# Kernel tuning notes

Hardware: AMD Instinct MI355X
Metric: run time of the kernel (lower is better)

Reference implementation:

```python
import jax, jax.numpy as jnp
import numpy as np

N_NODES = 50000
N_EDGES = 800000
HIDDEN = 128
MAX_Z = 1000
NUM_GRAPHS = 1000
NODES_PER_GRAPH = N_NODES // NUM_GRAPHS


def setup_inputs() -> dict:
    key = jax.random.key(0)
    ks = jax.random.split(key, 12)
    s = 1.0 / np.sqrt(HIDDEN)
    inp = {
        "z": jax.random.randint(ks[0], (N_NODES,), 0, MAX_Z),
        "edge_index": jax.random.randint(ks[1], (2, N_EDGES), 0, N_NODES),
        # sorted batch ids, 50 nodes per graph (SEAL-style subgraph batch)
        "batch": jnp.repeat(jnp.arange(NUM_GRAPHS), NODES_PER_GRAPH),
        "num_graphs": NUM_GRAPHS,
        "emb_table": jax.random.normal(ks[2], (MAX_Z, HIDDEN), jnp.float32),
        "w0": jax.random.normal(ks[3], (HIDDEN, HIDDEN), jnp.float32) * s,
        "b0": jnp.zeros((HIDDEN,), jnp.float32),
        "w1": jax.random.normal(ks[4], (HIDDEN, HIDDEN), jnp.float32) * s,
        "b1": jnp.zeros((HIDDEN,), jnp.float32),
        "w2": jax.random.normal(ks[5], (HIDDEN, HIDDEN), jnp.float32) * s,
        "b2": jnp.zeros((HIDDEN,), jnp.float32),
        "lin1_w": jax.random.normal(ks[6], (HIDDEN, HIDDEN), jnp.float32) * s,
        "lin1_b": jnp.zeros((HIDDEN,), jnp.float32),
        "lin2_w": jax.random.normal(ks[7], (HIDDEN, 1), jnp.float32) * s,
        "lin2_b": jnp.zeros((1,), jnp.float32),
    }
    return inp


def reference(z, edge_index, batch, num_graphs, emb_table, w0, b0, w1, b1, w2, b2,
              lin1_w, lin1_b, lin2_w, lin2_b):
    n = z.shape[0]
    # GCN symmetric normalization with self-loops (PyG gcn_norm, edge_weight=1)
    loops = jnp.arange(n)
    src = jnp.concatenate([edge_index[0], loops])
    dst = jnp.concatenate([edge_index[1], loops])
    ones = jnp.ones(src.shape[0], dtype=emb_table.dtype)
    deg = jax.ops.segment_sum(ones, dst, num_segments=n)
    dinv = jnp.where(deg > 0, jax.lax.rsqrt(deg), 0.0)
    norm = dinv[src] * dinv[dst]  # [E+N]

    def gcn_conv(x, W, b):
        h = x @ W  # linear transform first (bias added after aggregation)
        msg = h[src] * norm[:, None]  # gather + scale over edges
        return jax.ops.segment_sum(msg, dst, num_segments=n) + b

    x = emb_table[z]  # z embedding (z is 1-D -> no sum over dim 1)
    # dropout is identity in eval mode
    x = jax.nn.relu(gcn_conv(x, w0, b0))
    x = jax.nn.relu(gcn_conv(x, w1, b1))
    x = gcn_conv(x, w2, b2)

    # first occurrence of each batch id (batch is sorted per PyG convention)
    center = jax.ops.segment_min(jnp.arange(n), batch, num_segments=num_graphs)
    g = x[center] * x[center + 1]  # [G, H] pairwise link readout
    g = jax.nn.relu(g @ lin1_w + lin1_b)
    return g @ lin2_w + lin2_b  # [G, 1]
```

## Files before the change

### kernel.cpp

```cpp
#include <hip/hip_runtime.h>
#include <hip/hip_fp16.h>
#include <cstdint>
#include <cstddef>

#define H 128

typedef _Float16 f16x8 __attribute__((ext_vector_type(8)));
typedef float f32x4 __attribute__((ext_vector_type(4)));

__device__ inline float2 up2(unsigned u) {
    return __half22float2(*reinterpret_cast<const __half2*>(&u));
}
__device__ inline unsigned pk2(float a, float b) {
    __half2 h = __floats2half2_rn(a, b);
    return *reinterpret_cast<unsigned*>(&h);
}

__global__ void init_kernel(int* __restrict__ fill, int n,
                            const float* __restrict__ w0, const float* __restrict__ w1,
                            const float* __restrict__ w2, _Float16* __restrict__ wt) {
    int idx = blockIdx.x * 256 + threadIdx.x;
    if (idx < n) fill[idx] = 0;
    if (idx < 3 * H * H) {
        int m = idx >> 14;
        int c = (idx >> 7) & 127;
        int k = idx & 127;
        const float* W = (m == 0) ? w0 : (m == 1) ? w1 : w2;
        wt[idx] = (_Float16)W[k * H + c];
    }
}

__global__ __launch_bounds__(256) void fill_xcd(const int* __restrict__ src,
                                                const int* __restrict__ dst, int E,
                                                int* __restrict__ fill,
                                                unsigned short* __restrict__ csr_pad,
                                                int n, int rs) {
    int p = blockIdx.x & 7;
    int lo = p * rs;
    int hi = lo + rs; if (hi > n) hi = n;
    int nchunks = gridDim.x >> 3;
    int chunk = blockIdx.x >> 3;
    int stride = nchunks * 256;
    int E4 = E >> 2;
    const int4* dst4 = reinterpret_cast<const int4*>(dst);

    for (int q = chunk * 256 + threadIdx.x; q < E4; q += stride) {
        int4 d4 = dst4[q];
        int e = q * 4;
        if (d4.x >= lo && d4.x < hi) {
            int s = src[e];
            int pos = atomicAdd(&fill[d4.x], 1);
            if (pos < 64) csr_pad[(d4.x << 6) + pos] = (unsigned short)s;
        }
        if (d4.y >= lo && d4.y < hi) {
            int s = src[e + 1];
            int pos = atomicAdd(&fill[d4.y], 1);
            if (pos < 64) csr_pad[(d4.y << 6) + pos] = (unsigned short)s;
        }
        if (d4.z >= lo && d4.z < hi) {
            int s = src[e + 2];
            int pos = atomicAdd(&fill[d4.z], 1);
            if (pos < 64) csr_pad[(d4.z << 6) + pos] = (unsigned short)s;
        }
        if (d4.w >= lo && d4.w < hi) {
            int s = src[e + 3];
            int pos = atomicAdd(&fill[d4.w], 1);
            if (pos < 64) csr_pad[(d4.w << 6) + pos] = (unsigned short)s;
        }
    }
    if (blockIdx.x < 8) {
        int e = E4 * 4 + threadIdx.x;
        if (e < E) {
            int d = dst[e];
            if (d >= lo && d < hi) {
                int s = src[e];
                int pos = atomicAdd(&fill[d], 1);
                if (pos < 64) csr_pad[(d << 6) + pos] = (unsigned short)s;
            }
        }
    }
}

__global__ void post_fill(const int* __restrict__ fill, float* __restrict__ dinv,
                          const int* __restrict__ batch, int* __restrict__ sel, int n) {
    int i = blockIdx.x * 256 + threadIdx.x;
    if (i < n) {
        dinv[i] = rsqrtf((float)(fill[i] + 1));
        int b = batch[i];
        if (i == 0 || batch[i - 1] != b) {
            sel[2 * b] = i;
            sel[2 * b + 1] = (i + 1 < n) ? i + 1 : n - 1;
        }
    }
}


template<int MODE>
__global__ __launch_bounds__(256) void gemm_mfma(const void* __restrict__ Xv,
                                                 const int* __restrict__ z,
                                                 const _Float16* __restrict__ Wt,
                                                 unsigned* __restrict__ Yh, int n) {
    __shared__ _Float16 Wl[H * H];
    __shared__ _Float16 Cl[64 * H];
    int tid = threadIdx.x;

    {
        const uint4* src = reinterpret_cast<const uint4*>(Wt);
        #pragma unroll
        for (int it = 0; it < 8; ++it) {
            int idx = it * 256 + tid;
            int c = idx >> 4, s = idx & 15;
            unsigned boff = (unsigned)(c * 256 + s * 16) ^ ((unsigned)(c & 7) << 4);
            *reinterpret_cast<uint4*>(reinterpret_cast<char*>(Wl) + boff) = src[idx];
        }
    }

    int m0 = blockIdx.x * 64;
    int wid = tid >> 6, lane = tid & 63;
    int l15 = lane & 15, lhi = lane >> 4;
    int grow = m0 + wid * 16 + l15;
    bool rowok = grow < n;

    const float* xrow32 = nullptr;
    const _Float16* xrow16 = nullptr;
    if (MODE == 0) {
        const float* X = (const float*)Xv;
        int zr = rowok ? z[grow] : 0;
        xrow32 = X + (size_t)zr * H;
    } else {
        const _Float16* X = (const _Float16*)Xv;
        xrow16 = X + (size_t)(rowok ? grow : 0) * H;
    }

    unsigned braw[8];
    unsigned swz = (unsigned)(l15 & 7) << 4;
    #pragma unroll
    for (int ct = 0; ct < 8; ++ct) {
        int c = ct * 16 + l15;
        braw[ct] = (unsigned)(c * 256 + lhi * 16);
    }

    f32x4 acc[8];
    #pragma unroll
    for (int ct = 0; ct < 8; ++ct) acc[ct] = (f32x4){0.f, 0.f, 0.f, 0.f};

    __syncthreads();

    #pragma unroll
    for (int kb = 0; kb < 4; ++kb) {
        f16x8 a;
        if (MODE == 0) {
            const float* ap = xrow32 + kb * 32 + lhi * 8;
            float4 x0 = *reinterpret_cast<const float4*>(ap);
            float4 x1 = *reinterpret_cast<const float4*>(ap + 4);
            a[0] = (_Float16)x0.x; a[1] = (_Float16)x0.y;
            a[2] = (_Float16)x0.z; a[3] = (_Float16)x0.w;
            a[4] = (_Float16)x1.x; a[5] = (_Float16)x1.y;
            a[6] = (_Float16)x1.z; a[7] = (_Float16)x1.w;
        } else {
            a = *reinterpret_cast<const f16x8*>(xrow16 + kb * 32 + lhi * 8);
        }
        #pragma unroll
        for (int ct = 0; ct < 8; ++ct) {
            unsigned boff = (braw[ct] + (unsigned)(kb * 64)) ^ swz;
            f16x8 b = *reinterpret_cast<const f16x8*>(
                reinterpret_cast<const char*>(Wl) + boff);
            acc[ct] = __builtin_amdgcn_mfma_f32_16x16x32_f16(a, b, acc[ct], 0, 0, 0);
        }
    }

    _Float16* cw = Cl + wid * 16 * H;
    #pragma unroll
    for (int ct = 0; ct < 8; ++ct) {
        #pragma unroll
        for (int r = 0; r < 4; ++r) {
            int row = lhi * 4 + r;
            int col = ct * 16 + l15;
            cw[row * H + col] = (_Float16)acc[ct][r];
        }
    }
    int orow = lane >> 2, oseg = lane & 3;
    int growo = m0 + wid * 16 + orow;
    if (growo < n) {
        const uint4* cp = reinterpret_cast<const uint4*>(
            reinterpret_cast<const char*>(cw) + orow * 256 + oseg * 64);
        uint4* dp = reinterpret_cast<uint4*>(
            reinterpret_cast<char*>(Yh) + (size_t)growo * 256 + oseg * 64);
        dp[0] = cp[0]; dp[1] = cp[1]; dp[2] = cp[2]; dp[3] = cp[3];
    }
}


__device__ inline float4 agg_core(const unsigned* __restrict__ Hb,
                                  const unsigned short* __restrict__ csr_pad,
                                  const float* __restrict__ dinv,
                                  const float* __restrict__ bias,
                                  int node, int deg, float di,
                                  int lane, int half, int l32) {
    const uint2* Hu = reinterpret_cast<const uint2*>(Hb);
    float4 acc0 = make_float4(0.f, 0.f, 0.f, 0.f);
    float4 acc1 = make_float4(0.f, 0.f, 0.f, 0.f);
    float4 acc2 = make_float4(0.f, 0.f, 0.f, 0.f);
    float4 acc3 = make_float4(0.f, 0.f, 0.f, 0.f);
    if (half == 0) {
        float s = di * di;
        uint2 u = Hu[(size_t)node * 32 + l32];
        float4 bv = reinterpret_cast<const float4*>(bias)[l32];
        float2 f0 = up2(u.x), f1 = up2(u.y);
        acc0.x = bv.x + f0.x * s;
        acc0.y = bv.y + f0.y * s;
        acc0.z = bv.z + f1.x * s;
        acc0.w = bv.w + f1.y * s;
    }
    int beg = node << 6;
    int end = beg + deg;
    int j = beg + half;
    for (; j + 6 < end; j += 8) {
        int s0 = csr_pad[j];
        int s1 = csr_pad[j + 2];
        int s2 = csr_pad[j + 4];
        int s3 = csr_pad[j + 6];
        uint2 u0 = Hu[(size_t)s0 * 32 + l32];
        uint2 u1 = Hu[(size_t)s1 * 32 + l32];
        uint2 u2 = Hu[(size_t)s2 * 32 + l32];
        uint2 u3 = Hu[(size_t)s3 * 32 + l32];
        float n0 = dinv[s0] * di;
        float n1 = dinv[s1] * di;
        float n2 = dinv[s2] * di;
        float n3 = dinv[s3] * di;
        float2 a0 = up2(u0.x), b0 = up2(u0.y);
        float2 a1 = up2(u1.x), b1 = up2(u1.y);
        float2 a2 = up2(u2.x), b2 = up2(u2.y);
        float2 a3 = up2(u3.x), b3 = up2(u3.y);
        acc0.x = fmaf(a0.x, n0, acc0.x); acc0.y = fmaf(a0.y, n0, acc0.y);
        acc0.z = fmaf(b0.x, n0, acc0.z); acc0.w = fmaf(b0.y, n0, acc0.w);
        acc1.x = fmaf(a1.x, n1, acc1.x); acc1.y = fmaf(a1.y, n1, acc1.y);
        acc1.z = fmaf(b1.x, n1, acc1.z); acc1.w = fmaf(b1.y, n1, acc1.w);
        acc2.x = fmaf(a2.x, n2, acc2.x); acc2.y = fmaf(a2.y, n2, acc2.y);
        acc2.z = fmaf(b2.x, n2, acc2.z); acc2.w = fmaf(b2.y, n2, acc2.w);
        acc3.x = fmaf(a3.x, n3, acc3.x); acc3.y = fmaf(a3.y, n3, acc3.y);
        acc3.z = fmaf(b3.x, n3, acc3.z); acc3.w = fmaf(b3.y, n3, acc3.w);
    }
    for (; j < end; j += 2) {
        int s0 = csr_pad[j];
        uint2 u0 = Hu[(size_t)s0 * 32 + l32];
        float n0 = dinv[s0] * di;
        float2 a0 = up2(u0.x), b0 = up2(u0.y);
        acc0.x = fmaf(a0.x, n0, acc0.x); acc0.y = fmaf(a0.y, n0, acc0.y);
        acc0.z = fmaf(b0.x, n0, acc0.z); acc0.w = fmaf(b0.y, n0, acc0.w);
    }
    acc0.x += acc1.x + acc2.x + acc3.x;
    acc0.y += acc1.y + acc2.y + acc3.y;
    acc0.z += acc1.z + acc2.z + acc3.z;
    acc0.w += acc1.w + acc2.w + acc3.w;
    acc0.x += __shfl_xor(acc0.x, 32);
    acc0.y += __shfl_xor(acc0.y, 32);
    acc0.z += __shfl_xor(acc0.z, 32);
    acc0.w += __shfl_xor(acc0.w, 32);
    return acc0;
}

__global__ __launch_bounds__(256) void agg_f16(const unsigned* __restrict__ Hb,
                                               const int* __restrict__ degc,
                                               const unsigned short* __restrict__ csr_pad,
                                               const float* __restrict__ dinv,
                                               const float* __restrict__ bias,
                                               unsigned* __restrict__ Out, int n) {
    int node = blockIdx.x * 4 + (threadIdx.x >> 6);
    if (node >= n) return;
    int lane = threadIdx.x & 63;
    int half = lane >> 5, l32 = lane & 31;
    int deg = degc[node]; if (deg > 64) deg = 64;
    float di = dinv[node];
    float4 a = agg_core(Hb, csr_pad, dinv, bias, node, deg, di, lane, half, l32);
    if (half == 0) {
        a.x = fmaxf(a.x, 0.f); a.y = fmaxf(a.y, 0.f);
        a.z = fmaxf(a.z, 0.f); a.w = fmaxf(a.w, 0.f);
        uint2 pv; pv.x = pk2(a.x, a.y); pv.y = pk2(a.z, a.w);
        reinterpret_cast<uint2*>(Out)[(size_t)node * 32 + l32] = pv;
    }
}

__global__ __launch_bounds__(256) void agg_sel(const unsigned* __restrict__ Hb,
                                               const int* __restrict__ degc,
                                               const unsigned short* __restrict__ csr_pad,
                                               const float* __restrict__ dinv,
                                               const float* __restrict__ bias,
                                               const int* __restrict__ sel,
                                               float* __restrict__ Out, int nSel) {
    int idx = blockIdx.x * 4 + (threadIdx.x >> 6);
    if (idx >= nSel) return;
    int node = sel[idx];
    int lane = threadIdx.x & 63;
    int half = lane >> 5, l32 = lane & 31;
    int deg = degc[node]; if (deg > 64) deg = 64;
    float di = dinv[node];
    float4 a = agg_core(Hb, csr_pad, dinv, bias, node, deg, di, lane, half, l32);
    if (half == 0)
        reinterpret_cast<float4*>(Out)[(size_t)idx * 32 + l32] = a;
}


__global__ __launch_bounds__(128) void readout_kernel(const float* __restrict__ OSel,
                                                      const float* __restrict__ w1,
                                                      const float* __restrict__ b1,
                                                      const float* __restrict__ w2,
                                                      const float* __restrict__ b2,
                                                      float* __restrict__ out) {
    __shared__ float gv[H];
    __shared__ float red[H];
    int g = blockIdx.x;
    int c = threadIdx.x;
    gv[c] = OSel[(size_t)(2 * g) * H + c] * OSel[(size_t)(2 * g + 1) * H + c];
    __syncthreads();
    float acc = b1[c];
    #pragma unroll 8
    for (int k = 0; k < H; ++k)
        acc = fmaf(gv[k], w1[k * H + c], acc);
    acc = fmaxf(acc, 0.f);
    red[c] = acc * w2[c];
    __syncthreads();
    for (int off = 64; off > 0; off >>= 1) {
        if (c < off) red[c] += red[c + off];
        __syncthreads();
    }
    if (c == 0) out[g] = red[0] + b2[0];
}


static inline size_t align_up(size_t x) { return (x + 255) & ~(size_t)255; }

extern "C" void kernel_launch(void* const* d_in, const int* in_sizes, int n_in,
                              void* d_out, int out_size, void* d_ws, size_t ws_size,
                              hipStream_t stream) {
    const int n = in_sizes[0];
    const int E = in_sizes[1] / 2;
    const int G = out_size;

    const int*   z      = (const int*)d_in[0];
    const int*   ei     = (const int*)d_in[1];
    const int*   batch  = (const int*)d_in[2];
    const float* emb    = (const float*)d_in[4];
    const float* w0     = (const float*)d_in[5];
    const float* b0     = (const float*)d_in[6];
    const float* w1     = (const float*)d_in[7];
    const float* b1     = (const float*)d_in[8];
    const float* w2     = (const float*)d_in[9];
    const float* b2     = (const float*)d_in[10];
    const float* lin1_w = (const float*)d_in[11];
    const float* lin1_b = (const float*)d_in[12];
    const float* lin2_w = (const float*)d_in[13];
    const float* lin2_b = (const float*)d_in[14];

    const int* e_src = ei;
    const int* e_dst = ei + E;

    const int rs = (n + 7) / 8;

    char* p = (char*)d_ws;
    int*            fill     = (int*)p;            p += align_up((size_t)n * 4);
    int*            sel      = (int*)p;            p += align_up((size_t)2 * G * 4);
    unsigned short* csr_pad  = (unsigned short*)p; p += align_up((size_t)n * 64 * 2);
    float*          dinv     = (float*)p;          p += align_up((size_t)n * 4);
    _Float16*       wt       = (_Float16*)p;       p += align_up((size_t)3 * H * H * 2);
    unsigned*       hB       = (unsigned*)p;       p += align_up((size_t)n * 64 * 4);
    unsigned*       hA       = (unsigned*)p;       p += align_up((size_t)n * 64 * 4);
    float*          oSel     = (float*)p;          p += align_up((size_t)2 * G * H * 4);

    const int TB = 256;
    dim3 gN((n + TB - 1) / TB);

    init_kernel<<<gN, TB, 0, stream>>>(fill, n, w0, w1, w2, wt);
    fill_xcd<<<2048, 256, 0, stream>>>(e_src, e_dst, E, fill, csr_pad, n, rs);
    post_fill<<<gN, TB, 0, stream>>>(fill, dinv, batch, sel, n);

    dim3 gemm_grid((n + 63) / 64);
    dim3 agg_grid((n + 3) / 4);
    dim3 sel_grid((2 * G + 3) / 4);

    gemm_mfma<0><<<gemm_grid, 256, 0, stream>>>(emb, z, wt, hB, n);
    agg_f16<<<agg_grid, 256, 0, stream>>>(hB, fill, csr_pad, dinv, b0, hA, n);
    gemm_mfma<1><<<gemm_grid, 256, 0, stream>>>(hA, nullptr, wt + H * H, hB, n);
    agg_f16<<<agg_grid, 256, 0, stream>>>(hB, fill, csr_pad, dinv, b1, hA, n);
    gemm_mfma<1><<<gemm_grid, 256, 0, stream>>>(hA, nullptr, wt + 2 * H * H, hB, n);
    agg_sel<<<sel_grid, 256, 0, stream>>>(hB, fill, csr_pad, dinv, b2, sel, oSel, 2 * G);

    readout_kernel<<<G, 128, 0, stream>>>(oSel, lin1_w, lin1_b, lin2_w, lin2_b,
                                          (float*)d_out);
}
```

Baseline: 176.3 us.

## Bucket edges by destination partition before building padded CSR

Replaces the single-pass fill kernel, in which each of 8 partition groups rescanned the whole edge list, with a two-level radix-style bucketing. Edges are counted per block and partition, then prefix-scanned and scattered into a packed partition-sorted list. A final pass fills the padded CSR per partition while reading only that partition's edges. This removes the eightfold redundant reads of dst and the filtering branches, at the cost of three extra launches, a single-block scan, and an extra write plus read of an E-sized packed buffer.

Measured after the change: 183.0 us. 3.8% more time.

```diff
diff --git a/kernel.cpp b/kernel.cpp
--- a/kernel.cpp
+++ b/kernel.cpp
@@ -4,6 +4,7 @@
 #include <cstddef>
 
 #define H 128
+#define NBLK_A 256
 
 typedef _Float16 f16x8 __attribute__((ext_vector_type(8)));
 typedef float f32x4 __attribute__((ext_vector_type(4)));
@@ -16,68 +17,94 @@
     return *reinterpret_cast<unsigned*>(&h);
 }
 
-__global__ void init_kernel(int* __restrict__ fill, int n,
-                            const float* __restrict__ w0, const float* __restrict__ w1,
-                            const float* __restrict__ w2, _Float16* __restrict__ wt) {
-    int idx = blockIdx.x * 256 + threadIdx.x;
-    if (idx < n) fill[idx] = 0;
-    if (idx < 3 * H * H) {
+__global__ __launch_bounds__(256) void init_count(int* __restrict__ fill, int n,
+                                                  const float* __restrict__ w0,
+                                                  const float* __restrict__ w1,
+                                                  const float* __restrict__ w2,
+                                                  _Float16* __restrict__ wt,
+                                                  const int* __restrict__ dst, int E,
+                                                  int* __restrict__ cntA, int rs) {
+    int blk = blockIdx.x, tid = threadIdx.x;
+    int gid = blk * 256 + tid;
+    int gsz = NBLK_A * 256;
+    for (int i = gid; i < n; i += gsz) fill[i] = 0;
+    for (int idx = gid; idx < 3 * H * H; idx += gsz) {
         int m = idx >> 14;
         int c = (idx >> 7) & 127;
         int k = idx & 127;
         const float* W = (m == 0) ? w0 : (m == 1) ? w1 : w2;
         wt[idx] = (_Float16)W[k * H + c];
     }
-}
-
-__global__ __launch_bounds__(256) void fill_xcd(const int* __restrict__ src,
-                                                const int* __restrict__ dst, int E,
-                                                int* __restrict__ fill,
-                                                unsigned short* __restrict__ csr_pad,
-                                                int n, int rs) {
+    __shared__ int lc[8];
+    if (tid < 8) lc[tid] = 0;
+    __syncthreads();
+    int chunk = (E + NBLK_A - 1) / NBLK_A;
+    int beg = blk * chunk;
+    int end = beg + chunk; if (end > E) end = E;
+    for (int e = beg + tid; e < end; e += 256)
+        atomicAdd(&lc[dst[e] / rs], 1);
+    __syncthreads();
+    if (tid < 8) cntA[tid * NBLK_A + blk] = lc[tid];
+}
+
+__global__ __launch_bounds__(256) void scanA(int* __restrict__ cntA) {
+    __shared__ int sm[256];
+    int tid = threadIdx.x;
+    int base = tid * 8;
+    int v[8]; int s = 0;
+    #pragma unroll
+    for (int j = 0; j < 8; ++j) { v[j] = cntA[base + j]; s += v[j]; }
+    sm[tid] = s;
+    __syncthreads();
+    #pragma unroll
+    for (int off = 1; off < 256; off <<= 1) {
+        int t = (tid >= off) ? sm[tid - off] : 0;
+        __syncthreads();
+        sm[tid] += t;
+        __syncthreads();
+    }
+    int excl = sm[tid] - s;
+    #pragma unroll
+    for (int j = 0; j < 8; ++j) { cntA[base + j] = excl; excl += v[j]; }
+}
+
+__global__ __launch_bounds__(256) void writeA(const int* __restrict__ src,
+                                              const int* __restrict__ dst, int E,
+                                              const int* __restrict__ offA,
+                                              unsigned* __restrict__ elist, int rs) {
+    __shared__ int cur[8];
+    int blk = blockIdx.x, tid = threadIdx.x;
+    if (tid < 8) cur[tid] = offA[tid * NBLK_A + blk];
+    __syncthreads();
+    int chunk = (E + NBLK_A - 1) / NBLK_A;
+    int beg = blk * chunk;
+    int end = beg + chunk; if (end > E) end = E;
+    for (int e = beg + tid; e < end; e += 256) {
+        int d = dst[e];
+        int s = src[e];
+        int p = d / rs;
+        int dl = d - p * rs;
+        int slot = atomicAdd(&cur[p], 1);
+        elist[slot] = ((unsigned)s << 13) | (unsigned)dl;
+    }
+}
+
+__global__ __launch_bounds__(256) void fillB(const unsigned* __restrict__ elist,
+                                             const int* __restrict__ offA, int E,
+                                             int* __restrict__ fill,
+                                             unsigned short* __restrict__ csr_pad, int rs) {
     int p = blockIdx.x & 7;
-    int lo = p * rs;
-    int hi = lo + rs; if (hi > n) hi = n;
-    int nchunks = gridDim.x >> 3;
-    int chunk = blockIdx.x >> 3;
-    int stride = nchunks * 256;
-    int E4 = E >> 2;
-    const int4* dst4 = reinterpret_cast<const int4*>(dst);
-
-    for (int q = chunk * 256 + threadIdx.x; q < E4; q += stride) {
-        int4 d4 = dst4[q];
-        int e = q * 4;
-        if (d4.x >= lo && d4.x < hi) {
-            int s = src[e];
-            int pos = atomicAdd(&fill[d4.x], 1);
-            if (pos < 64) csr_pad[(d4.x << 6) + pos] = (unsigned short)s;
-        }
-        if (d4.y >= lo && d4.y < hi) {
-            int s = src[e + 1];
-            int pos = atomicAdd(&fill[d4.y], 1);
-            if (pos < 64) csr_pad[(d4.y << 6) + pos] = (unsigned short)s;
-        }
-        if (d4.z >= lo && d4.z < hi) {
-            int s = src[e + 2];
-            int pos = atomicAdd(&fill[d4.z], 1);
-            if (pos < 64) csr_pad[(d4.z << 6) + pos] = (unsigned short)s;
-        }
-        if (d4.w >= lo && d4.w < hi) {
-            int s = src[e + 3];
-            int pos = atomicAdd(&fill[d4.w], 1);
-            if (pos < 64) csr_pad[(d4.w << 6) + pos] = (unsigned short)s;
-        }
-    }
-    if (blockIdx.x < 8) {
-        int e = E4 * 4 + threadIdx.x;
-        if (e < E) {
-            int d = dst[e];
-            if (d >= lo && d < hi) {
-                int s = src[e];
-                int pos = atomicAdd(&fill[d], 1);
-                if (pos < 64) csr_pad[(d << 6) + pos] = (unsigned short)s;
-            }
-        }
+    int idx = blockIdx.x >> 3;
+    int start = offA[p * NBLK_A];
+    int end = (p == 7) ? E : offA[(p + 1) * NBLK_A];
+    int stride = (gridDim.x >> 3) * 256;
+    for (int j = start + idx * 256 + (int)threadIdx.x; j < end; j += stride) {
+        unsigned r = elist[j];
+        int dl = (int)(r & 8191u);
+        int s = (int)(r >> 13);
+        int d = p * rs + dl;
+        int pos = atomicAdd(&fill[d], 1);
+        if (pos < 64) csr_pad[(d << 6) + pos] = (unsigned short)s;
     }
 }
 
@@ -360,6 +387,8 @@
     char* p = (char*)d_ws;
     int*            fill     = (int*)p;            p += align_up((size_t)n * 4);
     int*            sel      = (int*)p;            p += align_up((size_t)2 * G * 4);
+    int*            cntA     = (int*)p;            p += align_up((size_t)8 * NBLK_A * 4);
+    unsigned*       elist    = (unsigned*)p;       p += align_up((size_t)E * 4);
     unsigned short* csr_pad  = (unsigned short*)p; p += align_up((size_t)n * 64 * 2);
     float*          dinv     = (float*)p;          p += align_up((size_t)n * 4);
     _Float16*       wt       = (_Float16*)p;       p += align_up((size_t)3 * H * H * 2);
@@ -370,8 +399,10 @@
     const int TB = 256;
     dim3 gN((n + TB - 1) / TB);
 
-    init_kernel<<<gN, TB, 0, stream>>>(fill, n, w0, w1, w2, wt);
-    fill_xcd<<<2048, 256, 0, stream>>>(e_src, e_dst, E, fill, csr_pad, n, rs);
+    init_count<<<NBLK_A, TB, 0, stream>>>(fill, n, w0, w1, w2, wt, e_dst, E, cntA, rs);
+    scanA<<<1, TB, 0, stream>>>(cntA);
+    writeA<<<NBLK_A, TB, 0, stream>>>(e_src, e_dst, E, cntA, elist, rs);
+    fillB<<<2048, TB, 0, stream>>>(elist, cntA, E, fill, csr_pad, rs);
     post_fill<<<gN, TB, 0, stream>>>(fill, dinv, batch, sel, n);
 
     dim3 gemm_grid((n + 63) / 64);
```
